# Kernel optimization log

Hardware: AMD Instinct MI355X
Metric: run time of the kernel (lower is better)

The kernel has to match this reference:

```python
import jax, jax.numpy as jnp
import numpy as np

B, N, DIM, H = 4, 128, 512, 8
EPS = 1e-5

def _lin(k, fan_in, fan_out):
    kw, kb = jax.random.split(k)
    w = jax.random.normal(kw, (fan_in, fan_out), jnp.float32) * 0.02
    b = jax.random.normal(kb, (fan_out,), jnp.float32) * 0.02
    return w, b

def setup_inputs() -> dict:
    key = jax.random.key(0)
    ks = jax.random.split(key, 12)
    node_features = jax.random.normal(ks[0], (B, N, DIM), jnp.float32)
    edge_features = jax.random.normal(ks[1], (B, N, N, DIM), jnp.float32)
    adjacency_weights = jax.random.uniform(ks[2], (B, N, N), jnp.float32)
    Wn_w, Wn_b = _lin(ks[3], DIM, DIM)
    We1_w, We1_b = _lin(ks[4], 3 * DIM, DIM)
    We2_w, We2_b = _lin(ks[5], DIM, H)
    Wm_w, Wm_b = _lin(ks[6], DIM, DIM)
    Wu1_w, Wu1_b = _lin(ks[7], 3 * DIM, DIM)
    Wu2_w, Wu2_b = _lin(ks[8], DIM, DIM)
    Wo_w, Wo_b = _lin(ks[9], DIM, DIM)
    ln_g = jnp.ones((DIM,), jnp.float32)
    ln_b = jnp.zeros((DIM,), jnp.float32)
    return dict(node_features=node_features, edge_features=edge_features,
                adjacency_weights=adjacency_weights,
                Wn_w=Wn_w, Wn_b=Wn_b, We1_w=We1_w, We1_b=We1_b,
                We2_w=We2_w, We2_b=We2_b, Wm_w=Wm_w, Wm_b=Wm_b,
                Wu1_w=Wu1_w, Wu1_b=Wu1_b, Wu2_w=Wu2_w, Wu2_b=Wu2_b,
                Wo_w=Wo_w, Wo_b=Wo_b, ln_g=ln_g, ln_b=ln_b)

def _layernorm(x, g, b):
    mu = jnp.mean(x, axis=-1, keepdims=True)
    var = jnp.var(x, axis=-1, keepdims=True)
    return (x - mu) * jax.lax.rsqrt(var + EPS) * g + b

def reference(node_features, edge_features, adjacency_weights,
              Wn_w, Wn_b, We1_w, We1_b, We2_w, We2_b, Wm_w, Wm_b,
              Wu1_w, Wu1_b, Wu2_w, Wu2_b, Wo_w, Wo_b, ln_g, ln_b):
    b, n, d = node_features.shape
    h = node_features @ Wn_w + Wn_b                       # (B,N,D)
    h_i = jnp.broadcast_to(h[:, :, None, :], (b, n, n, d))
    h_j = jnp.broadcast_to(h[:, None, :, :], (b, n, n, d))
    edge_input = jnp.concatenate([h_i, h_j, edge_features], axis=-1)  # (B,N,N,3D)
    # edge attention MLP
    e = jax.nn.leaky_relu(edge_input @ We1_w + We1_b, negative_slope=0.2)
    attn = e @ We2_w + We2_b                              # (B,N,N,H)
    attn = jax.nn.softmax(attn, axis=2)                   # softmax over j
    attn = attn * adjacency_weights[..., None]
    # messages: W_msg applied to h_j == W_msg(h) broadcast; aggregate with mean attn
    messages = h @ Wm_w + Wm_b                            # (B,N,D)
    attn_mean = jnp.mean(attn, axis=-1)                   # (B,N,N)
    aggregated = jnp.einsum('bij,bjd->bid', attn_mean, messages)
    updated_nodes = _layernorm(node_features + (aggregated @ Wo_w + Wo_b), ln_g, ln_b)
    # edge update MLP (exact GELU as in torch default)
    u = jax.nn.gelu(edge_input @ Wu1_w + Wu1_b, approximate=False)
    updated_edges = edge_features + (u @ Wu2_w + Wu2_b)
    return updated_nodes, updated_edges
```

## Files before the change

kernel.cpp:

```cpp
#include <hip/hip_runtime.h>
#include <hip/hip_bf16.h>


typedef __bf16  bf16x8 __attribute__((ext_vector_type(8)));
typedef float   f32x4  __attribute__((ext_vector_type(4)));
typedef __hip_bfloat16 bfloat;

#define AS1 __attribute__((address_space(1)))
#define AS3 __attribute__((address_space(3)))

__device__ __forceinline__ void g2l16(const void* g, void* l) {
  __builtin_amdgcn_global_load_lds((AS1 void*)g, (AS3 void*)l, 16, 0, 0);
}

__device__ __forceinline__ float ldf(const void* p, size_t i, int f) {
  return f ? ((const float*)p)[i] : __bfloat162float(((const bfloat*)p)[i]);
}
__device__ __forceinline__ void stf(void* p, size_t i, float v, int f) {
  if (f) ((float*)p)[i] = v;
  else   ((bfloat*)p)[i] = __float2bfloat16(v);
}

__device__ __forceinline__ float gelu_f(float x) {
  float y = 0.7978845608028654f * (x + 0.044715f * x * x * x);
  float e = __expf(2.0f * y);
  float t = 1.0f - 2.0f / (e + 1.0f);
  return 0.5f * x * (1.0f + t);
}

__global__ __launch_bounds__(256) void detect_dtype(const unsigned short* nu, int* flag) {
  __shared__ int bad;
  if (threadIdx.x == 0) bad = 0;
  __syncthreads();
  int local = 0;
  for (int i = threadIdx.x; i < 4096; i += 256) {
    int ex = (nu[i] >> 7) & 0xFF;
    if (ex >= 0xC0) local = 1;
  }
  if (local) atomicOr(&bad, 1);
  __syncthreads();
  if (threadIdx.x == 0) *flag = bad;
}

__global__ __launch_bounds__(256) void cvt_edge(const float* E, const int* flag, void* dout) {
  if (*flag == 0) return;
  const int e = blockIdx.x & 7;
  const int x = blockIdx.x >> 3;
  const int m = x >> 5;
  const int h = (x >> 4) & 1;
  const int s = x & 15;
  const int c = 2 * e + 16 * m + h;
  const int t = threadIdx.x;
  const int rloc = s * 4 + (t >> 6);
  const int c8 = t & 63;
  const float* src = E + ((size_t)c * 64 + rloc) * 512 + (size_t)c8 * 8;
  f32x4 lo = *(const f32x4*)src;
  f32x4 hi = *(const f32x4*)(src + 4);
  bf16x8 v;
  v[0] = (__bf16)lo[0]; v[1] = (__bf16)lo[1]; v[2] = (__bf16)lo[2]; v[3] = (__bf16)lo[3];
  v[4] = (__bf16)hi[0]; v[5] = (__bf16)hi[1]; v[6] = (__bf16)hi[2]; v[7] = (__bf16)hi[3];
  char* eb = (char*)dout + 1048576;
  *(bf16x8*)(eb + (size_t)c * 131072 + (size_t)rloc * 1024 + (size_t)c8 * 16) = v;
}

__global__ __launch_bounds__(256) void transpose3(const void* We1, const void* Wu1,
                                                  const void* Wu2, const int* flag,
                                                  bfloat* WtA, bfloat* WtB, bfloat* WtC) {
  const int f = *flag;
  int idx = blockIdx.x * 256 + threadIdx.x;
  int m = idx >> 18;
  int r = idx & 262143;
  int n = r >> 9, k = r & 511;
  size_t si = (size_t)k * 512 + n;
  float v;
  bfloat* dst;
  if (m == 0)      { v = ldf(We1, 524288 + si, f); dst = WtA; }
  else if (m == 1) { v = ldf(Wu1, 524288 + si, f); dst = WtB; }
  else             { v = ldf(Wu2, si, f);          dst = WtC; }
  dst[(size_t)n * 512 + k] = __float2bfloat16(v);
}

__global__ __launch_bounds__(256) void small_gemm(const void* A, int amode, const void* W,
                                                  size_t woff, const void* bias,
                                                  const int* flag, float* out) {
  const int f = *flag;
  const int af = amode ? 1 : f;
  __shared__ float sA[4][512];
  const int t = threadIdx.x;
  const int r0 = blockIdx.x * 4;
  for (int idx = t; idx < 2048; idx += 256)
    sA[idx >> 9][idx & 511] = ldf(A, (size_t)(r0 + (idx >> 9)) * 512 + (idx & 511), af);
  __syncthreads();
  float acc0[4] = {0.f, 0.f, 0.f, 0.f}, acc1[4] = {0.f, 0.f, 0.f, 0.f};
#pragma unroll 4
  for (int k = 0; k < 512; ++k) {
    float w0 = ldf(W, woff + (size_t)k * 512 + t, f);
    float w1 = ldf(W, woff + (size_t)k * 512 + t + 256, f);
#pragma unroll
    for (int r = 0; r < 4; ++r) {
      acc0[r] += sA[r][k] * w0;
      acc1[r] += sA[r][k] * w1;
    }
  }
  float b0 = bias ? ldf(bias, t, f) : 0.f;
  float b1 = bias ? ldf(bias, t + 256, f) : 0.f;
#pragma unroll
  for (int r = 0; r < 4; ++r) {
    out[(size_t)(r0 + r) * 512 + t] = acc0[r] + b0;
    out[(size_t)(r0 + r) * 512 + t + 256] = acc1[r] + b1;
  }
}

__global__ __launch_bounds__(256) void fused5(const float* h, const void* We1, const void* We1b,
                                              const void* Wu1, const void* Wu1b, const void* Wm,
                                              const void* Wmb, const int* flag, float* P1,
                                              float* Q1, float* P2, float* Q2, float* msgv) {
  const int f = *flag;
  const void* W;
  size_t woff = 0;
  const void* bias = nullptr;
  float* out;
  switch (blockIdx.y) {
    case 0:  W = We1; bias = We1b; out = P1; break;
    case 1:  W = We1; woff = 262144; out = Q1; break;
    case 2:  W = Wu1; bias = Wu1b; out = P2; break;
    case 3:  W = Wu1; woff = 262144; out = Q2; break;
    default: W = Wm;  bias = Wmb;  out = msgv; break;
  }
  __shared__ float sA[4][512];
  const int t = threadIdx.x;
  const int r0 = blockIdx.x * 4;
  for (int idx = t; idx < 2048; idx += 256)
    sA[idx >> 9][idx & 511] = h[(size_t)(r0 + (idx >> 9)) * 512 + (idx & 511)];
  __syncthreads();
  float acc0[4] = {0.f, 0.f, 0.f, 0.f}, acc1[4] = {0.f, 0.f, 0.f, 0.f};
#pragma unroll 4
  for (int k = 0; k < 512; ++k) {
    float w0 = ldf(W, woff + (size_t)k * 512 + t, f);
    float w1 = ldf(W, woff + (size_t)k * 512 + t + 256, f);
#pragma unroll
    for (int r = 0; r < 4; ++r) {
      acc0[r] += sA[r][k] * w0;
      acc1[r] += sA[r][k] * w1;
    }
  }
  float b0 = bias ? ldf(bias, t, f) : 0.f;
  float b1 = bias ? ldf(bias, t + 256, f) : 0.f;
#pragma unroll
  for (int r = 0; r < 4; ++r) {
    out[(size_t)(r0 + r) * 512 + t] = acc0[r] + b0;
    out[(size_t)(r0 + r) * 512 + t + 256] = acc1[r] + b1;
  }
}

__global__ __launch_bounds__(256) void k3_edge_mlp(const void* E, const bfloat* WtA,
                                                   const bfloat* WtB, const float* P1,
                                                   const float* Q1, const float* P2,
                                                   const float* Q2, const void* We2,
                                                   const int* flag, float* logits4, void* dout) {
  const int f = *flag;
  __shared__ __align__(16) char smem[32768];
  char* sA = smem;
  char* sB = smem + 16384;
  f32x4 acc[4][4];
#pragma unroll
  for (int mi = 0; mi < 4; ++mi)
#pragma unroll
    for (int ni = 0; ni < 4; ++ni) acc[mi][ni] = (f32x4){0.f, 0.f, 0.f, 0.f};

  const int idx0 = blockIdx.x;
  const int bm = (idx0 >> 6) * 8 + (idx0 & 7);
  const int bn = (idx0 >> 3) & 7;
  const bool attn = bn < 4;
  const bfloat* Bg = attn ? WtA + (size_t)bn * 65536 : WtB + (size_t)(bn - 4) * 65536;
  const bfloat* Eb = (const bfloat*)E;
  const char* eb = (const char*)dout + 1048576;

  const int t = threadIdx.x;
  const int lane = t & 63;
  const int wave = t >> 6;
  const int wrow = wave >> 1, wcol = wave & 1;
  const int l15 = lane & 15;
  const int q = lane >> 4;

  for (int kt = 0; kt < 8; ++kt) {
    __syncthreads();
    const int k0 = kt * 64;
#pragma unroll
    for (int c = 0; c < 4; ++c) {
      const int L = c * 256 + t;
      const int row = L >> 3;
      const int g = (L & 7) ^ ((row >> 0) & 7);
      char* dstb = sB + (c * 256 + wave * 64) * 16;
      char* dsta = sA + (c * 256 + wave * 64) * 16;
      g2l16(Bg + (size_t)row * 512 + k0 + g * 8, dstb);
      const int gr = bm * 128 + row;
      if (f) {
        g2l16(eb + (size_t)(gr >> 6) * 131072 + (size_t)(gr & 63) * 1024 +
                  (size_t)(k0 + g * 8) * 2,
              dsta);
      } else {
        g2l16(Eb + (size_t)gr * 512 + k0 + g * 8, dsta);
      }
    }
    __syncthreads();
#pragma unroll
    for (int kk = 0; kk < 2; ++kk) {
      bf16x8 afr[4], bfr[4];
#pragma unroll
      for (int mi = 0; mi < 4; ++mi) {
        const int r = wrow * 64 + mi * 16 + l15;
        afr[mi] = *(const bf16x8*)(sA + (size_t)r * 128 + (((kk * 4 + q) ^ (r & 7)) * 16));
      }
#pragma unroll
      for (int ni = 0; ni < 4; ++ni) {
        const int r = wcol * 64 + ni * 16 + l15;
        bfr[ni] = *(const bf16x8*)(sB + (size_t)r * 128 + (((kk * 4 + q) ^ (r & 7)) * 16));
      }
#pragma unroll
      for (int mi = 0; mi < 4; ++mi)
#pragma unroll
        for (int ni = 0; ni < 4; ++ni)
          acc[mi][ni] =
              __builtin_amdgcn_mfma_f32_16x16x32_bf16(afr[mi], bfr[ni], acc[mi][ni], 0, 0, 0);
    }
  }

  const int b = bm >> 7;
  const int blockcol = (attn ? bn : (bn - 4)) * 128;
  const float* P = attn ? P1 : P2;
  const float* Qm = attn ? Q1 : Q2;
  float pv[4];
#pragma unroll
  for (int ni = 0; ni < 4; ++ni)
    pv[ni] = P[(size_t)bm * 512 + blockcol + wcol * 64 + ni * 16 + l15];

  if (!attn) {
    __syncthreads();
    bfloat* simg = (bfloat*)smem;
#pragma unroll
    for (int mi = 0; mi < 4; ++mi)
#pragma unroll
      for (int rr = 0; rr < 4; ++rr) {
        const int j = wrow * 64 + mi * 16 + q * 4 + rr;
#pragma unroll
        for (int ni = 0; ni < 4; ++ni) {
          const int cc = wcol * 64 + ni * 16 + l15;
          const int c = blockcol + cc;
          float x = acc[mi][ni][rr] + pv[ni] + Qm[((size_t)b * 128 + j) * 512 + c];
          *(bfloat*)(smem + (size_t)j * 256 + (((cc >> 3) ^ (j & 15)) * 16) + (cc & 7) * 2) =
              __float2bfloat16(gelu_f(x));
        }
      }
    (void)simg;
    __syncthreads();
    char* ubase = (char*)dout + (f ? (1048576 + 65536) : 524288);
    const size_t blkstride = f ? 131072 : 65536;
#pragma unroll
    for (int rd = 0; rd < 8; ++rd) {
      const int j = rd * 16 + (t >> 4);
      const int ch = t & 15;
      f32x4 v = *(const f32x4*)(smem + (size_t)j * 256 + ((ch ^ (j & 15)) * 16));
      const size_t m = (size_t)bm * 128 + j;
      *(f32x4*)(ubase + (m >> 6) * blkstride + (m & 63) * 1024 + (size_t)blockcol * 2 +
                (size_t)ch * 16) = v;
    }
  } else {
    float w2[4][8];
#pragma unroll
    for (int ni = 0; ni < 4; ++ni) {
      const int c = blockcol + wcol * 64 + ni * 16 + l15;
#pragma unroll
      for (int hh = 0; hh < 8; ++hh) w2[ni][hh] = ldf(We2, (size_t)c * 8 + hh, f);
    }
    __syncthreads();
    float* sp = (float*)smem;
#pragma unroll
    for (int mi = 0; mi < 4; ++mi)
#pragma unroll
      for (int rr = 0; rr < 4; ++rr) {
        const int j = wrow * 64 + mi * 16 + q * 4 + rr;
        float e4[4];
#pragma unroll
        for (int ni = 0; ni < 4; ++ni) {
          const int c = blockcol + wcol * 64 + ni * 16 + l15;
          float x = acc[mi][ni][rr] + pv[ni] + Qm[((size_t)b * 128 + j) * 512 + c];
          e4[ni] = (x >= 0.f) ? x : 0.2f * x;
        }
#pragma unroll
        for (int hh = 0; hh < 8; ++hh) {
          float s = e4[0] * w2[0][hh] + e4[1] * w2[1][hh] + e4[2] * w2[2][hh] + e4[3] * w2[3][hh];
          s += __shfl_xor(s, 1);
          s += __shfl_xor(s, 2);
          s += __shfl_xor(s, 4);
          s += __shfl_xor(s, 8);
          if (l15 == 0) sp[(wcol * 128 + j) * 8 + hh] = s;
        }
      }
    __syncthreads();
    {
      const int j = t >> 1;
      const int h0 = (t & 1) * 4;
      f32x4 v;
#pragma unroll
      for (int k = 0; k < 4; ++k)
        v[k] = sp[j * 8 + h0 + k] + sp[(128 + j) * 8 + h0 + k];
      *(f32x4*)(logits4 + (((size_t)bn * 512 + bm) * 128 + j) * 8 + h0) = v;
    }
  }
}

__global__ __launch_bounds__(512) void k6_edge_out(const bfloat* WtC, const void* Wu2b,
                                                   const void* E, const int* flag, void* dout) {
  const int f = *flag;
  __shared__ __align__(16) char smem[36864];
  char* sA = smem;
  char* sB = smem + 4096;
  f32x4 acc[2][8];
#pragma unroll
  for (int mi = 0; mi < 2; ++mi)
#pragma unroll
    for (int ni = 0; ni < 8; ++ni) acc[mi][ni] = (f32x4){0.f, 0.f, 0.f, 0.f};

  const int e = blockIdx.x & 7;
  const int x = blockIdx.x >> 3;
  const int bm = 2 * e + 16 * (x >> 1) + (x & 1);
  const int t = threadIdx.x;
  const int lane = t & 63;
  const int wave = t >> 6;
  const int wm = wave >> 2, wn = wave & 3;
  const int l15 = lane & 15;
  const int q = lane >> 4;
  const size_t r0 = (size_t)bm * 64;
  const char* ua = (const char*)dout +
                   (f ? (1048576 + (size_t)bm * 131072 + 65536) : (524288 + (size_t)bm * 65536));

  for (int kt = 0; kt < 16; ++kt) {
    __syncthreads();
    const int k0 = kt * 32;
    if (t < 256) {
      const int row = t >> 2;
      const int gseg = (t & 3) ^ ((row >> 1) & 3);
      g2l16(ua + (size_t)row * 1024 + (size_t)(k0 + gseg * 8) * 2, sA + wave * 64 * 16);
    }
#pragma unroll
    for (int c = 0; c < 4; ++c) {
      const int idx = c * 512 + t;
      const int row = idx >> 2;
      const int gseg = (idx & 3) ^ ((row >> 1) & 3);
      g2l16(WtC + (size_t)row * 512 + k0 + gseg * 8, sB + (c * 512 + wave * 64) * 16);
    }
    __syncthreads();
    bf16x8 afr[2], bfr[8];
#pragma unroll
    for (int mi = 0; mi < 2; ++mi) {
      const int r = wm * 32 + mi * 16 + l15;
      afr[mi] = *(const bf16x8*)(sA + ((size_t)r * 32 + (q ^ ((r >> 1) & 3)) * 8) * 2);
    }
#pragma unroll
    for (int ni = 0; ni < 8; ++ni) {
      const int r = wn * 128 + ni * 16 + l15;
      bfr[ni] = *(const bf16x8*)(sB + ((size_t)r * 32 + (q ^ ((r >> 1) & 3)) * 8) * 2);
    }
#pragma unroll
    for (int mi = 0; mi < 2; ++mi)
#pragma unroll
      for (int ni = 0; ni < 8; ++ni)
        acc[mi][ni] = __builtin_amdgcn_mfma_f32_16x16x32_bf16(afr[mi], bfr[ni], acc[mi][ni], 0, 0, 0);
  }
  float wb[8];
#pragma unroll
  for (int ni = 0; ni < 8; ++ni) wb[ni] = ldf(Wu2b, wn * 128 + ni * 16 + l15, f);
  const bfloat* eres = (const bfloat*)((const char*)dout + 1048576 + (size_t)bm * 131072);
#pragma unroll
  for (int mi = 0; mi < 2; ++mi)
#pragma unroll
    for (int rr = 0; rr < 4; ++rr) {
      const int j = wm * 32 + mi * 16 + q * 4 + rr;
#pragma unroll
      for (int ni = 0; ni < 8; ++ni) {
        const int c = wn * 128 + ni * 16 + l15;
        float r = f ? __bfloat162float(eres[(size_t)j * 512 + c])
                    : __bfloat162float(((const bfloat*)E)[(r0 + j) * 512 + c]);
        acc[mi][ni][rr] += wb[ni] + r;
      }
    }
  __syncthreads();
#pragma unroll
  for (int mi = 0; mi < 2; ++mi)
#pragma unroll
    for (int rr = 0; rr < 4; ++rr) {
      const int j = wm * 32 + mi * 16 + q * 4 + rr;
      const size_t row = r0 + j;
#pragma unroll
      for (int ni = 0; ni < 8; ++ni) {
        const int c = wn * 128 + ni * 16 + l15;
        stf(dout, 262144 + row * 512 + c, acc[mi][ni][rr], f);
      }
    }
}

__global__ __launch_bounds__(128) void softmax_mean(const float* logits4, const void* adj,
                                                    const int* flag, float* amean) {
  const int f = *flag;
  const int bi = blockIdx.x;
  const int j = threadIdx.x;
  __shared__ float red[128];
  float macc = 0.f;
  for (int hh = 0; hh < 8; ++hh) {
    float x = 0.f;
#pragma unroll
    for (int s = 0; s < 4; ++s)
      x += logits4[(((size_t)s * 512 + bi) * 128 + j) * 8 + hh];
    red[j] = x;
    __syncthreads();
    for (int s = 64; s > 0; s >>= 1) {
      if (j < s) red[j] = fmaxf(red[j], red[j + s]);
      __syncthreads();
    }
    float mx = red[0];
    __syncthreads();
    float ex = __expf(x - mx);
    red[j] = ex;
    __syncthreads();
    for (int s = 64; s > 0; s >>= 1) {
      if (j < s) red[j] += red[j + s];
      __syncthreads();
    }
    float sum = red[0];
    __syncthreads();
    macc += ex / sum;
  }
  amean[(size_t)bi * 128 + j] = macc * 0.125f * ldf(adj, (size_t)bi * 128 + j, f);
}

__global__ __launch_bounds__(256) void node_fused(const float* amean, const float* msg,
                                                  const void* Wo, const void* Wob,
                                                  const void* node, const void* lng,
                                                  const void* lnb, const int* flag, void* dout) {
  const int f = *flag;
  const int bi = blockIdx.x;
  const int b = bi >> 7;
  const int t = threadIdx.x;
  __shared__ float am[128];
  __shared__ float sAgg[512];
  __shared__ float red[256];
  if (t < 128) am[t] = amean[(size_t)bi * 128 + t];
  __syncthreads();
  float a0 = 0.f, a1 = 0.f;
#pragma unroll 4
  for (int jj = 0; jj < 128; ++jj) {
    const float* mr = msg + ((size_t)b * 128 + jj) * 512;
    a0 += am[jj] * mr[t];
    a1 += am[jj] * mr[t + 256];
  }
  sAgg[t] = a0;
  sAgg[t + 256] = a1;
  __syncthreads();
  float v0 = 0.f, v1 = 0.f;
#pragma unroll 4
  for (int k = 0; k < 512; ++k) {
    float a = sAgg[k];
    v0 += a * ldf(Wo, (size_t)k * 512 + t, f);
    v1 += a * ldf(Wo, (size_t)k * 512 + t + 256, f);
  }
  v0 += ldf(Wob, t, f) + ldf(node, (size_t)bi * 512 + t, f);
  v1 += ldf(Wob, t + 256, f) + ldf(node, (size_t)bi * 512 + t + 256, f);
  red[t] = v0 + v1;
  __syncthreads();
  for (int s = 128; s > 0; s >>= 1) {
    if (t < s) red[t] += red[t + s];
    __syncthreads();
  }
  float mean = red[0] * (1.f / 512.f);
  __syncthreads();
  red[t] = (v0 - mean) * (v0 - mean) + (v1 - mean) * (v1 - mean);
  __syncthreads();
  for (int s = 128; s > 0; s >>= 1) {
    if (t < s) red[t] += red[t + s];
    __syncthreads();
  }
  float var = red[0] * (1.f / 512.f);
  float inv = rsqrtf(var + 1e-5f);
  stf(dout, (size_t)bi * 512 + t, (v0 - mean) * inv * ldf(lng, t, f) + ldf(lnb, t, f), f);
  stf(dout, (size_t)bi * 512 + t + 256,
      (v1 - mean) * inv * ldf(lng, t + 256, f) + ldf(lnb, t + 256, f), f);
}

extern "C" void kernel_launch(void* const* d_in, const int* in_sizes, int n_in, void* d_out,
                              int out_size, void* d_ws, size_t ws_size, hipStream_t stream) {
  (void)in_sizes; (void)n_in; (void)out_size; (void)ws_size;
  const void* node = d_in[0];
  const void* edge = d_in[1];
  const void* adj = d_in[2];
  const void* Wn_w = d_in[3];
  const void* Wn_b = d_in[4];
  const void* We1_w = d_in[5];
  const void* We1_b = d_in[6];
  const void* We2_w = d_in[7];
  const void* Wm_w = d_in[9];
  const void* Wm_b = d_in[10];
  const void* Wu1_w = d_in[11];
  const void* Wu1_b = d_in[12];
  const void* Wu2_w = d_in[13];
  const void* Wu2_b = d_in[14];
  const void* Wo_w = d_in[15];
  const void* Wo_b = d_in[16];
  const void* ln_g = d_in[17];
  const void* ln_b = d_in[18];

  char* w = (char*)d_ws;
  int* flag = (int*)w;        w += 256;
  float* h = (float*)w;       w += 262144 * 4;
  float* P1 = (float*)w;      w += 262144 * 4;
  float* Q1 = (float*)w;      w += 262144 * 4;
  float* P2 = (float*)w;      w += 262144 * 4;
  float* Q2 = (float*)w;      w += 262144 * 4;
  float* msg = (float*)w;     w += 262144 * 4;
  float* logits4 = (float*)w; w += (size_t)4 * 524288 * 4;
  float* amean = (float*)w;   w += 65536 * 4;
  bfloat* WtA = (bfloat*)w;   w += 262144 * 2;
  bfloat* WtB = (bfloat*)w;   w += 262144 * 2;
  bfloat* WtC = (bfloat*)w;   w += 262144 * 2;

  detect_dtype<<<1, 256, 0, stream>>>((const unsigned short*)node, flag);
  cvt_edge<<<16384, 256, 0, stream>>>((const float*)edge, flag, d_out);
  transpose3<<<3072, 256, 0, stream>>>(We1_w, Wu1_w, Wu2_w, flag, WtA, WtB, WtC);
  small_gemm<<<128, 256, 0, stream>>>(node, 0, Wn_w, 0, Wn_b, flag, h);
  fused5<<<dim3(128, 5), 256, 0, stream>>>(h, We1_w, We1_b, Wu1_w, Wu1_b, Wm_w, Wm_b, flag,
                                           P1, Q1, P2, Q2, msg);
  k3_edge_mlp<<<4096, 256, 0, stream>>>(edge, WtA, WtB, P1, Q1, P2, Q2, We2_w, flag,
                                        logits4, d_out);
  softmax_mean<<<512, 128, 0, stream>>>(logits4, adj, flag, amean);
  node_fused<<<512, 256, 0, stream>>>(amean, msg, Wo_w, Wo_b, node, ln_g, ln_b, flag, d_out);
  k6_edge_out<<<1024, 512, 0, stream>>>(WtC, Wu2_b, edge, flag, d_out);
}
```

Measured before the change: 874.9 us.

## Triple-buffer edge MLP K-loop and compute attention head projection with MFMA

The edge MLP kernel's K loop changes from synchronous 64-wide tiles into 32-wide tiles with a three-stage global-to-LDS pipeline, using vmcnt waits so loads overlap MFMA work. The attention epilogue's per-lane We2 dot products with shuffle reductions are replaced by writing the leaky-ReLU activations to LDS as bf16 and running a small MFMA against a padded We2 tile. This aims to hide memory latency and cut shuffle and ALU overhead in the epilogue. In exchange, LDS use grows to 52KB, which may reduce occupancy, and the second GEMM now rounds activations to bf16.

```diff
diff --git a/kernel.cpp b/kernel.cpp
--- a/kernel.cpp
+++ b/kernel.cpp
@@ -159,9 +159,7 @@
                                                    const float* Q2, const void* We2,
                                                    const int* flag, float* logits4, void* dout) {
   const int f = *flag;
-  __shared__ __align__(16) char smem[32768];
-  char* sA = smem;
-  char* sB = smem + 16384;
+  __shared__ __align__(16) char smem[53248];
   f32x4 acc[4][4];
 #pragma unroll
   for (int mi = 0; mi < 4; ++mi)
@@ -182,52 +180,72 @@
   const int wrow = wave >> 1, wcol = wave & 1;
   const int l15 = lane & 15;
   const int q = lane >> 4;
-
-  for (int kt = 0; kt < 8; ++kt) {
-    __syncthreads();
-    const int k0 = kt * 64;
-#pragma unroll
-    for (int c = 0; c < 4; ++c) {
-      const int L = c * 256 + t;
-      const int row = L >> 3;
-      const int g = (L & 7) ^ ((row >> 0) & 7);
-      char* dstb = sB + (c * 256 + wave * 64) * 16;
-      char* dsta = sA + (c * 256 + wave * 64) * 16;
-      g2l16(Bg + (size_t)row * 512 + k0 + g * 8, dstb);
-      const int gr = bm * 128 + row;
-      if (f) {
-        g2l16(eb + (size_t)(gr >> 6) * 131072 + (size_t)(gr & 63) * 1024 +
-                  (size_t)(k0 + g * 8) * 2,
-              dsta);
-      } else {
-        g2l16(Eb + (size_t)gr * 512 + k0 + g * 8, dsta);
-      }
-    }
-    __syncthreads();
-#pragma unroll
-    for (int kk = 0; kk < 2; ++kk) {
-      bf16x8 afr[4], bfr[4];
-#pragma unroll
-      for (int mi = 0; mi < 4; ++mi) {
-        const int r = wrow * 64 + mi * 16 + l15;
-        afr[mi] = *(const bf16x8*)(sA + (size_t)r * 128 + (((kk * 4 + q) ^ (r & 7)) * 16));
-      }
-#pragma unroll
-      for (int ni = 0; ni < 4; ++ni) {
-        const int r = wcol * 64 + ni * 16 + l15;
-        bfr[ni] = *(const bf16x8*)(sB + (size_t)r * 128 + (((kk * 4 + q) ^ (r & 7)) * 16));
-      }
-#pragma unroll
-      for (int mi = 0; mi < 4; ++mi)
-#pragma unroll
-        for (int ni = 0; ni < 4; ++ni)
-          acc[mi][ni] =
-              __builtin_amdgcn_mfma_f32_16x16x32_bf16(afr[mi], bfr[ni], acc[mi][ni], 0, 0, 0);
-    }
+  const int blockcol = (attn ? bn : (bn - 4)) * 128;
+
+  const int row0 = t >> 2, p0 = t & 3, g0 = p0 ^ (row0 & 3);
+  const int row1 = 64 + row0, g1 = p0 ^ (row1 & 3);
+  const char* srcB0 = (const char*)Bg + ((size_t)row0 * 512 + g0 * 8) * 2;
+  const char* srcB1 = (const char*)Bg + ((size_t)row1 * 512 + g1 * 8) * 2;
+  const char* srcA0;
+  const char* srcA1;
+  const int gr0 = bm * 128 + row0, gr1 = gr0 + 64;
+  if (f) {
+    srcA0 = eb + (size_t)(gr0 >> 6) * 131072 + (size_t)(gr0 & 63) * 1024 + (size_t)g0 * 16;
+    srcA1 = eb + (size_t)(gr1 >> 6) * 131072 + (size_t)(gr1 & 63) * 1024 + (size_t)g1 * 16;
+  } else {
+    srcA0 = (const char*)Eb + ((size_t)gr0 * 512 + g0 * 8) * 2;
+    srcA1 = (const char*)Eb + ((size_t)gr1 * 512 + g1 * 8) * 2;
+  }
+  const int dst0 = wave * 1024;
+  const int dst1 = 4096 + wave * 1024;
+
+  auto stage = [&](int kt2, int sel2) {
+    char* dA = smem + sel2 * 8192;
+    char* dB = smem + 24576 + sel2 * 8192;
+    const int koff = kt2 * 64;
+    g2l16(srcA0 + koff, dA + dst0);
+    g2l16(srcA1 + koff, dA + dst1);
+    g2l16(srcB0 + koff, dB + dst0);
+    g2l16(srcB1 + koff, dB + dst1);
+  };
+
+  stage(0, 0);
+  stage(1, 1);
+
+  if (attn) {
+    for (int idx = t; idx < 2048; idx += 256) {
+      const int n = idx >> 7, k = idx & 127;
+      float v = (n < 8) ? ldf(We2, (size_t)(blockcol + k) * 8 + n, f) : 0.f;
+      *(bfloat*)(smem + 49152 + (size_t)n * 256 + (((k >> 3) ^ n) * 16) + (k & 7) * 2) =
+          __float2bfloat16(v);
+    }
+  }
+
+  const int fA = (wrow * 64 + l15) * 64 + ((q ^ (l15 & 3)) * 16);
+  const int fB = (wcol * 64 + l15) * 64 + ((q ^ (l15 & 3)) * 16);
+
+#pragma unroll
+  for (int kt = 0; kt < 16; ++kt) {
+    if (kt < 15) asm volatile("s_waitcnt vmcnt(4)" ::: "memory");
+    else         asm volatile("s_waitcnt vmcnt(0)" ::: "memory");
+    __builtin_amdgcn_s_barrier();
+    if (kt < 14) stage(kt + 2, (kt + 2) % 3);
+    const char* A = smem + (kt % 3) * 8192;
+    const char* B = smem + 24576 + (kt % 3) * 8192;
+    bf16x8 afr[4], bfr[4];
+#pragma unroll
+    for (int mi = 0; mi < 4; ++mi) afr[mi] = *(const bf16x8*)(A + fA + mi * 1024);
+#pragma unroll
+    for (int ni = 0; ni < 4; ++ni) bfr[ni] = *(const bf16x8*)(B + fB + ni * 1024);
+#pragma unroll
+    for (int mi = 0; mi < 4; ++mi)
+#pragma unroll
+      for (int ni = 0; ni < 4; ++ni)
+        acc[mi][ni] =
+            __builtin_amdgcn_mfma_f32_16x16x32_bf16(afr[mi], bfr[ni], acc[mi][ni], 0, 0, 0);
   }
 
   const int b = bm >> 7;
-  const int blockcol = (attn ? bn : (bn - 4)) * 128;
   const float* P = attn ? P1 : P2;
   const float* Qm = attn ? Q1 : Q2;
   float pv[4];
@@ -235,9 +253,9 @@
   for (int ni = 0; ni < 4; ++ni)
     pv[ni] = P[(size_t)bm * 512 + blockcol + wcol * 64 + ni * 16 + l15];
 
+  __syncthreads();
+
   if (!attn) {
-    __syncthreads();
-    bfloat* simg = (bfloat*)smem;
 #pragma unroll
     for (int mi = 0; mi < 4; ++mi)
 #pragma unroll
@@ -252,7 +270,6 @@
               __float2bfloat16(gelu_f(x));
         }
       }
-    (void)simg;
     __syncthreads();
     char* ubase = (char*)dout + (f ? (1048576 + 65536) : 524288);
     const size_t blkstride = f ? 131072 : 65536;
@@ -266,47 +283,44 @@
                 (size_t)ch * 16) = v;
     }
   } else {
-    float w2[4][8];
-#pragma unroll
-    for (int ni = 0; ni < 4; ++ni) {
-      const int c = blockcol + wcol * 64 + ni * 16 + l15;
-#pragma unroll
-      for (int hh = 0; hh < 8; ++hh) w2[ni][hh] = ldf(We2, (size_t)c * 8 + hh, f);
-    }
-    __syncthreads();
-    float* sp = (float*)smem;
 #pragma unroll
     for (int mi = 0; mi < 4; ++mi)
 #pragma unroll
       for (int rr = 0; rr < 4; ++rr) {
         const int j = wrow * 64 + mi * 16 + q * 4 + rr;
-        float e4[4];
 #pragma unroll
         for (int ni = 0; ni < 4; ++ni) {
-          const int c = blockcol + wcol * 64 + ni * 16 + l15;
+          const int cc = wcol * 64 + ni * 16 + l15;
+          const int c = blockcol + cc;
           float x = acc[mi][ni][rr] + pv[ni] + Qm[((size_t)b * 128 + j) * 512 + c];
-          e4[ni] = (x >= 0.f) ? x : 0.2f * x;
-        }
-#pragma unroll
-        for (int hh = 0; hh < 8; ++hh) {
-          float s = e4[0] * w2[0][hh] + e4[1] * w2[1][hh] + e4[2] * w2[2][hh] + e4[3] * w2[3][hh];
-          s += __shfl_xor(s, 1);
-          s += __shfl_xor(s, 2);
-          s += __shfl_xor(s, 4);
-          s += __shfl_xor(s, 8);
-          if (l15 == 0) sp[(wcol * 128 + j) * 8 + hh] = s;
+          float e4 = (x >= 0.f) ? x : 0.2f * x;
+          *(bfloat*)(smem + (size_t)j * 256 + (((cc >> 3) ^ (j & 15)) * 16) + (cc & 7) * 2) =
+              __float2bfloat16(e4);
         }
       }
     __syncthreads();
-    {
-      const int j = t >> 1;
-      const int h0 = (t & 1) * 4;
-      f32x4 v;
-#pragma unroll
-      for (int k = 0; k < 4; ++k)
-        v[k] = sp[j * 8 + h0 + k] + sp[(128 + j) * 8 + h0 + k];
-      *(f32x4*)(logits4 + (((size_t)bn * 512 + bm) * 128 + j) * 8 + h0) = v;
-    }
+    f32x4 acc2[2];
+    acc2[0] = (f32x4){0.f, 0.f, 0.f, 0.f};
+    acc2[1] = (f32x4){0.f, 0.f, 0.f, 0.f};
+    const int jb = wave * 32;
+#pragma unroll
+    for (int ks = 0; ks < 4; ++ks) {
+      const int gA = ((ks * 4 + q) ^ l15) * 16;
+      bf16x8 a0 = *(const bf16x8*)(smem + (size_t)(jb + l15) * 256 + gA);
+      bf16x8 a1 = *(const bf16x8*)(smem + (size_t)(jb + 16 + l15) * 256 + gA);
+      bf16x8 bb = *(const bf16x8*)(smem + 49152 + (size_t)l15 * 256 + gA);
+      acc2[0] = __builtin_amdgcn_mfma_f32_16x16x32_bf16(a0, bb, acc2[0], 0, 0, 0);
+      acc2[1] = __builtin_amdgcn_mfma_f32_16x16x32_bf16(a1, bb, acc2[1], 0, 0, 0);
+    }
+#pragma unroll
+    for (int mi2 = 0; mi2 < 2; ++mi2)
+#pragma unroll
+      for (int rr = 0; rr < 4; ++rr) {
+        if (l15 < 8) {
+          const int j = jb + mi2 * 16 + q * 4 + rr;
+          logits4[(((size_t)bn * 512 + bm) * 128 + j) * 8 + l15] = acc2[mi2][rr];
+        }
+      }
   }
 }
 
```

New measurement: 752.8 us. 14.0% less time.
